# Kernel optimization log

Measured on AMD Instinct MI355X. Metric: run time of the kernel, lower is better.

## Reference

```python
import jax, jax.numpy as jnp
import numpy as np

N, E, D, L, B, T = 50000, 600000, 128, 7, 512, 10
ATOM_DIMS = [119, 4, 12, 12, 10, 6, 6, 2, 2]
BOND_DIMS = [5, 6, 2]
MSG_EPS = 1e-7   # GENConv message epsilon
BN_EPS = 1e-5    # torch BatchNorm1d eps


def _offsets(dims):
    return jnp.asarray(np.concatenate([[0], np.cumsum(dims[:-1])]), dtype=jnp.int32)


def setup_inputs():
    key = jax.random.key(0)
    k = lambda i: jax.random.fold_in(key, i)
    x = jnp.stack([jax.random.randint(k(i), (N,), 0, d) for i, d in enumerate(ATOM_DIMS)], axis=1)
    edge_attr = jnp.stack([jax.random.randint(k(100 + i), (E,), 0, d) for i, d in enumerate(BOND_DIMS)], axis=1)
    edge_index = jax.random.randint(k(200), (2, E), 0, N)
    batch = jnp.sort(jax.random.randint(k(201), (N,), 0, B))
    atom_table = 0.1 * jax.random.normal(k(300), (sum(ATOM_DIMS), D), jnp.float32)
    bond_table = 0.1 * jax.random.normal(k(301), (sum(BOND_DIMS), D), jnp.float32)
    norm_gamma = jnp.ones((L, D), jnp.float32)
    norm_beta = jnp.zeros((L, D), jnp.float32)
    t = 0.1 * jnp.ones((L,), jnp.float32)
    mlp_w1 = 0.05 * jax.random.normal(k(302), (L, D, 2 * D), jnp.float32)
    mlp_b1 = jnp.zeros((L, 2 * D), jnp.float32)
    mlp_bng = jnp.ones((L, 2 * D), jnp.float32)
    mlp_bnb = jnp.zeros((L, 2 * D), jnp.float32)
    mlp_w2 = 0.05 * jax.random.normal(k(303), (L, 2 * D, D), jnp.float32)
    mlp_b2 = jnp.zeros((L, D), jnp.float32)
    pred_w = 0.05 * jax.random.normal(k(304), (D, T), jnp.float32)
    pred_b = jnp.zeros((T,), jnp.float32)
    return dict(x=x, edge_index=edge_index, edge_attr=edge_attr, batch=batch,
                atom_offsets=_offsets(ATOM_DIMS), bond_offsets=_offsets(BOND_DIMS),
                atom_table=atom_table, bond_table=bond_table,
                norm_gamma=norm_gamma, norm_beta=norm_beta, t=t,
                mlp_w1=mlp_w1, mlp_b1=mlp_b1, mlp_bng=mlp_bng, mlp_bnb=mlp_bnb,
                mlp_w2=mlp_w2, mlp_b2=mlp_b2, pred_w=pred_w, pred_b=pred_b)


def _batchnorm(z, gamma, beta):
    # training-mode BatchNorm1d: batch stats, biased variance
    mu = z.mean(0)
    var = z.var(0)
    return (z - mu) * jax.lax.rsqrt(var + BN_EPS) * gamma + beta


def _genconv(h, ea, src, dst, t, w1, b1, g1, bt1, w2, b2):
    # GENConv: message = relu(x_j + edge_attr) + eps; softmax aggregation with temperature t
    msg = jax.nn.relu(h[src] + ea) + MSG_EPS                 # [E, D]
    logits = msg * t
    m = jax.ops.segment_max(logits, dst, num_segments=N)     # [N, D]
    m = jax.lax.stop_gradient(jnp.where(jnp.isfinite(m), m, 0.0))
    e = jnp.exp(logits - m[dst])
    denom = jax.ops.segment_sum(e, dst, num_segments=N)
    alpha = e / (denom[dst] + 1e-16)
    aggr = jax.ops.segment_sum(msg * alpha, dst, num_segments=N)  # [N, D]
    out = h + aggr                                           # update: x_r + aggr
    z = _batchnorm(out @ w1 + b1, g1, bt1)                   # MLP: D -> 2D (BN, ReLU) -> D
    return jax.nn.relu(z) @ w2 + b2


def reference(x, edge_index, edge_attr, batch, atom_offsets, bond_offsets,
              atom_table, bond_table, norm_gamma, norm_beta, t,
              mlp_w1, mlp_b1, mlp_bng, mlp_bnb, mlp_w2, mlp_b2, pred_w, pred_b):
    h = atom_table[x + atom_offsets[None, :]].sum(1)               # [N, D] AtomEncoder
    ea = bond_table[edge_attr + bond_offsets[None, :]].sum(1)      # [E, D] BondEncoder
    src, dst = edge_index[0], edge_index[1]
    # first layer: bare conv
    h = _genconv(h, ea, src, dst, t[0], mlp_w1[0], mlp_b1[0], mlp_bng[0], mlp_bnb[0], mlp_w2[0], mlp_b2[0])
    # remaining layers: res+ blocks (norm -> act -> conv -> residual); dropout=0
    for i in range(1, L):
        r = jax.nn.relu(_batchnorm(h, norm_gamma[i], norm_beta[i]))
        r = _genconv(r, ea, src, dst, t[i], mlp_w1[i], mlp_b1[i], mlp_bng[i], mlp_bnb[i], mlp_w2[i], mlp_b2[i])
        h = h + r
    h = _batchnorm(h, norm_gamma[0], norm_beta[0])                 # layers[0].norm
    # global mean pool over graphs
    sums = jax.ops.segment_sum(h, batch, num_segments=B)
    cnts = jax.ops.segment_sum(jnp.ones((N,), h.dtype), batch, num_segments=B)
    graph_emb = sums / jnp.maximum(cnts, 1.0)[:, None]
    return graph_emb @ pred_w + pred_b                             # [B, T]
```

## Files before the change

### kernel.cpp

```cpp
#include <hip/hip_runtime.h>
#include <hip/hip_bf16.h>

#define N_NODES 50000
#define N_EDGES 600000
#define D 128
#define D2 256
#define NGRAPH 512
#define NTARGET 10
#define NSB 49
#define NSLOT 32

static constexpr float MSG_EPS_F = 1e-7f;
static constexpr float BN_EPS_F  = 1e-5f;

typedef _Float16 half8 __attribute__((ext_vector_type(8)));
typedef _Float16 half4v __attribute__((ext_vector_type(4)));
typedef float f32x4 __attribute__((ext_vector_type(4)));
#define MFMA16(a, b, c) __builtin_amdgcn_mfma_f32_16x16x32_f16(a, b, c, 0, 0, 0)

__global__ __launch_bounds__(256) void k_encode(
    const int* __restrict__ x, const int* __restrict__ aoff,
    const float* __restrict__ atab, float* __restrict__ h,
    _Float16* __restrict__ hh, int* __restrict__ deg) {
  int tid = blockIdx.x * 256 + threadIdx.x;
  if (tid < N_NODES) deg[tid] = 0;
  int n = tid >> 5, f4 = (tid & 31) << 2;
  if (n >= N_NODES) return;
  float4 acc = make_float4(0.f, 0.f, 0.f, 0.f);
#pragma unroll
  for (int i = 0; i < 9; ++i) {
    int row = x[n * 9 + i] + aoff[i];
    float4 v = *(const float4*)&atab[row * D + f4];
    acc.x += v.x; acc.y += v.y; acc.z += v.z; acc.w += v.w;
  }
  *(float4*)&h[(size_t)n * D + f4] = acc;
  half4v o = {(_Float16)acc.x, (_Float16)acc.y, (_Float16)acc.z, (_Float16)acc.w};
  *(half4v*)&hh[(size_t)n * D + f4] = o;
}

__global__ __launch_bounds__(128) void k_combo(
    const int* __restrict__ boff, const float* __restrict__ btab,
    _Float16* __restrict__ comboh) {
  int c = blockIdx.x, t = threadIdx.x;
  int a0 = c / 12, a1 = (c % 12) / 2, a2 = c % 2;
  comboh[c * D + t] = (_Float16)(btab[(boff[0] + a0) * D + t] +
                                 btab[(boff[1] + a1) * D + t] +
                                 btab[(boff[2] + a2) * D + t]);
}

__global__ __launch_bounds__(256) void k_packW(
    const float* __restrict__ w1, const float* __restrict__ w2,
    _Float16* __restrict__ w1p, _Float16* __restrict__ w2p) {
  int t = blockIdx.x * 256 + threadIdx.x;
  if (t < 7 * 4096) {
    int lane = t & 63, ntAll = (t >> 6) & 15, kc = (t >> 10) & 3, l = t >> 12;
    int q = lane >> 4, c = ntAll * 16 + (lane & 15);
    int kbase = kc * 32 + q * 8;
    const float* W = w1 + (size_t)l * D * D2;
    half8 v;
#pragma unroll
    for (int j = 0; j < 8; ++j) v[j] = (_Float16)W[(size_t)(kbase + j) * D2 + c];
    *(half8*)&w1p[(size_t)t * 8] = v;
  } else {
    int u = t - 7 * 4096;
    if (u < 7 * 4096) {
      int lane = u & 63, nt = (u >> 6) & 7, kcAll = (u >> 9) & 7, l = u >> 12;
      int q = lane >> 4, c = nt * 16 + (lane & 15);
      int kbase = kcAll * 32 + q * 8;
      const float* W = w2 + (size_t)l * D2 * D;
      half8 v;
#pragma unroll
      for (int j = 0; j < 8; ++j) v[j] = (_Float16)W[(size_t)(kbase + j) * D + c];
      *(half8*)&w2p[(size_t)u * 8] = v;
    }
  }
}

__global__ __launch_bounds__(256) void k_degree(
    const int* __restrict__ ei, int* __restrict__ deg) {
  int e = blockIdx.x * 256 + threadIdx.x;
  if (e >= N_EDGES) return;
  atomicAdd(&deg[ei[N_EDGES + e]], 1);
}

__global__ __launch_bounds__(1024) void k_scan1(
    const int* __restrict__ deg, int* __restrict__ excl, int* __restrict__ bsum) {
  __shared__ int tmp[1024];
  int t = threadIdx.x, i = blockIdx.x * 1024 + t;
  int v = (i < N_NODES) ? deg[i] : 0;
  tmp[t] = v;
  __syncthreads();
  for (int off = 1; off < 1024; off <<= 1) {
    int add = (t >= off) ? tmp[t - off] : 0;
    __syncthreads();
    tmp[t] += add;
    __syncthreads();
  }
  if (i < N_NODES) excl[i] = tmp[t] - v;
  if (t == 1023) bsum[blockIdx.x] = tmp[1023];
}

__global__ __launch_bounds__(64) void k_scan2(int* __restrict__ bsum) {
  __shared__ int s[64];
  int t = threadIdx.x;
  int v = (t < NSB) ? bsum[t] : 0;
  s[t] = v;
  __syncthreads();
  for (int off = 1; off < 64; off <<= 1) {
    int add = (t >= off) ? s[t - off] : 0;
    __syncthreads();
    s[t] += add;
    __syncthreads();
  }
  if (t < NSB) bsum[t] = s[t] - v;
}

__global__ __launch_bounds__(256) void k_scan3(
    const int* __restrict__ excl, const int* __restrict__ bsum,
    int* __restrict__ rowptr, int* __restrict__ cursor) {
  int i = blockIdx.x * 256 + threadIdx.x;
  if (i < N_NODES) {
    int v = excl[i] + bsum[i >> 10];
    rowptr[i] = v;
    cursor[i] = v;
  }
  if (i == N_NODES) rowptr[N_NODES] = N_EDGES;
}

__global__ __launch_bounds__(256) void k_scatter(
    const int* __restrict__ ei, const int* __restrict__ eattr,
    int* __restrict__ cursor, int* __restrict__ payload) {
  int e = blockIdx.x * 256 + threadIdx.x;
  if (e >= N_EDGES) return;
  int src = ei[e], dst = ei[N_EDGES + e];
  int cid = eattr[e * 3 + 0] * 12 + eattr[e * 3 + 1] * 2 + eattr[e * 3 + 2];
  int pos = atomicAdd(&cursor[dst], 1);
  payload[pos] = (src << 6) | cid;
}

__global__ __launch_bounds__(256) void k_gbounds(
    const int* __restrict__ batch, int* __restrict__ gstart,
    int* __restrict__ hist) {
  int n = blockIdx.x * 256 + threadIdx.x;
  if (n < 64) hist[n] = 0;
  if (n >= N_NODES) return;
  int b0 = batch[n];
  int b1 = (n + 1 < N_NODES) ? batch[n + 1] : NGRAPH;
  for (int bb = b0 + 1; bb <= b1; ++bb) gstart[bb] = n + 1;
  if (n == 0)
    for (int bb = 0; bb <= b0; ++bb) gstart[bb] = 0;
}

__global__ __launch_bounds__(256) void k_hist(
    const int* __restrict__ deg, int* __restrict__ hist) {
  __shared__ int lh[64];
  int tid = threadIdx.x;
  if (tid < 64) lh[tid] = 0;
  __syncthreads();
  int n = blockIdx.x * 256 + tid;
  if (n < N_NODES) atomicAdd(&lh[min(deg[n], 63)], 1);
  __syncthreads();
  if (tid < 64 && lh[tid]) atomicAdd(&hist[tid], lh[tid]);
}

__global__ __launch_bounds__(64) void k_scanhist(
    const int* __restrict__ hist, int* __restrict__ cursor2) {
  __shared__ int s[64];
  int t = threadIdx.x;
  int v = hist[t];
  s[t] = v;
  __syncthreads();
  for (int off = 1; off < 64; off <<= 1) {
    int add = (t >= off) ? s[t - off] : 0;
    __syncthreads();
    s[t] += add;
    __syncthreads();
  }
  cursor2[t] = s[t] - v;
}

__global__ __launch_bounds__(256) void k_permscatter(
    const int* __restrict__ deg, int* __restrict__ cursor2,
    int* __restrict__ perm) {
  __shared__ int lh[64], lbase[64];
  int tid = threadIdx.x;
  if (tid < 64) lh[tid] = 0;
  __syncthreads();
  int n = blockIdx.x * 256 + tid;
  int b = -1, lpos = 0;
  if (n < N_NODES) {
    b = min(deg[n], 63);
    lpos = atomicAdd(&lh[b], 1);
  }
  __syncthreads();
  if (tid < 64 && lh[tid]) lbase[tid] = atomicAdd(&cursor2[tid], lh[tid]);
  __syncthreads();
  if (b >= 0) perm[lbase[b] + lpos] = n;
}

__global__ __launch_bounds__(128) void k_bncoef(
    const float* __restrict__ statHsPrev, const float* __restrict__ gamma,
    const float* __restrict__ beta, float* __restrict__ bncoef, int identity) {
  int t = threadIdx.x;
  if (identity) {
    bncoef[t] = 1.f;
    bncoef[128 + t] = 0.f;
    return;
  }
  float s = 0.f, sq = 0.f;
#pragma unroll
  for (int sl = 0; sl < NSLOT; ++sl) {
    s += statHsPrev[sl * 256 + t];
    sq += statHsPrev[sl * 256 + 128 + t];
  }
  const float invN = 1.0f / (float)N_NODES;
  float mu = s * invN, var = sq * invN - mu * mu;
  float isg = rsqrtf(var + BN_EPS_F) * gamma[t];
  bncoef[t] = isg;
  bncoef[128 + t] = beta[t] - mu * isg;
}

__global__ __launch_bounds__(256) void k_aggrx(
    const _Float16* __restrict__ hh, const int* __restrict__ rowptr,
    const int* __restrict__ payload, const _Float16* __restrict__ comboh,
    const int* __restrict__ perm, const float* __restrict__ tptr, int l,
    const float* __restrict__ bncoef, float negcap, _Float16* __restrict__ xh) {
  int tid = blockIdx.x * 256 + threadIdx.x;
  int gi = tid >> 4, f8 = (tid & 15) << 3;
  if (gi >= N_NODES) return;
  int dst = perm[gi];
  float tv = tptr[l];
  float a[8], bb[8];
  *(float4*)&a[0] = *(const float4*)&bncoef[f8];
  *(float4*)&a[4] = *(const float4*)&bncoef[f8 + 4];
  *(float4*)&bb[0] = *(const float4*)&bncoef[128 + f8];
  *(float4*)&bb[4] = *(const float4*)&bncoef[128 + f8 + 4];
  int s = rowptr[dst], e = rowptr[dst + 1];
  float den[8], S[8];
#pragma unroll
  for (int j = 0; j < 8; ++j) { den[j] = 0.f; S[j] = 0.f; }
  int i = s;
  for (; i + 1 < e; i += 2) {
    int p0 = payload[i], p1 = payload[i + 1];
    half8 h0 = *(const half8*)&hh[(size_t)(p0 >> 6) * D + f8];
    half8 h1v = *(const half8*)&hh[(size_t)(p1 >> 6) * D + f8];
    half8 c0 = *(const half8*)&comboh[(p0 & 63) * D + f8];
    half8 c1 = *(const half8*)&comboh[(p1 & 63) * D + f8];
#pragma unroll
    for (int j = 0; j < 8; ++j) {
      float r0 = fmaxf(fmaf((float)h0[j], a[j], bb[j]), negcap);
      float r1 = fmaxf(fmaf((float)h1v[j], a[j], bb[j]), negcap);
      float m0 = fmaxf(r0 + (float)c0[j], 0.f) + MSG_EPS_F;
      float m1 = fmaxf(r1 + (float)c1[j], 0.f) + MSG_EPS_F;
      float e0 = __expf(m0 * tv), e1 = __expf(m1 * tv);
      den[j] += e0 + e1;
      S[j] += m0 * e0 + m1 * e1;
    }
  }
  if (i < e) {
    int p0 = payload[i];
    half8 h0 = *(const half8*)&hh[(size_t)(p0 >> 6) * D + f8];
    half8 c0 = *(const half8*)&comboh[(p0 & 63) * D + f8];
#pragma unroll
    for (int j = 0; j < 8; ++j) {
      float r0 = fmaxf(fmaf((float)h0[j], a[j], bb[j]), negcap);
      float m0 = fmaxf(r0 + (float)c0[j], 0.f) + MSG_EPS_F;
      float e0 = __expf(m0 * tv);
      den[j] += e0;
      S[j] += m0 * e0;
    }
  }
  half8 hd = *(const half8*)&hh[(size_t)dst * D + f8];
  half8 o;
#pragma unroll
  for (int j = 0; j < 8; ++j) {
    float rd = fmaxf(fmaf((float)hd[j], a[j], bb[j]), negcap);
    o[j] = (_Float16)(rd + S[j] / (den[j] + 1e-16f));
  }
  *(half8*)&xh[(size_t)dst * D + f8] = o;
}

__global__ __launch_bounds__(256) void k_gemm1(
    const _Float16* __restrict__ xh, const _Float16* __restrict__ w1p,
    const float* __restrict__ b1, _Float16* __restrict__ z1h,
    float* __restrict__ stat1s) {
  __shared__ __align__(16) _Float16 Af[512 * 8];
  int tid = threadIdx.x;
  int row0 = blockIdx.x * 32;
  int slot = blockIdx.x & (NSLOT - 1);

#pragma unroll
  for (int s0 = 0; s0 < 2; ++s0) {
    int s = s0 * 256 + tid;
    int kc = s >> 7, mt = (s >> 6) & 1, l2 = s & 63;
    int row = row0 + mt * 16 + (l2 & 15);
    int kb = kc * 32 + ((l2 >> 4) << 3);
    half8 v;
    if (row < N_NODES) {
      v = *(const half8*)&xh[(size_t)row * D + kb];
    } else {
#pragma unroll
      for (int j = 0; j < 8; ++j) v[j] = (_Float16)0.f;
    }
    *(half8*)&Af[s * 8] = v;
  }
  __syncthreads();

  int wv = tid >> 6, ln = tid & 63;
  f32x4 acc[2][4];
#pragma unroll
  for (int i = 0; i < 2; ++i)
#pragma unroll
    for (int j = 0; j < 4; ++j) acc[i][j] = (f32x4){0.f, 0.f, 0.f, 0.f};

#pragma unroll
  for (int kc = 0; kc < 4; ++kc) {
    half8 a0 = *(half8*)&Af[((kc * 2 + 0) * 64 + ln) * 8];
    half8 a1 = *(half8*)&Af[((kc * 2 + 1) * 64 + ln) * 8];
#pragma unroll
    for (int nt = 0; nt < 4; ++nt) {
      int ntAll = wv * 4 + nt;
      half8 b = *(const half8*)&w1p[((size_t)(kc * 16 + ntAll) * 64 + ln) * 8];
      acc[0][nt] = MFMA16(a0, b, acc[0][nt]);
      acc[1][nt] = MFMA16(a1, b, acc[1][nt]);
    }
  }
  int lq = ln >> 4, lc = ln & 15;
  float cs[4], cq[4];
#pragma unroll
  for (int nt = 0; nt < 4; ++nt) { cs[nt] = 0.f; cq[nt] = 0.f; }
#pragma unroll
  for (int nt = 0; nt < 4; ++nt) {
    int col = (wv * 4 + nt) * 16 + lc;
    float bias = b1[col];
#pragma unroll
    for (int mt = 0; mt < 2; ++mt) {
      int rbase = row0 + mt * 16 + lq * 4;
#pragma unroll
      for (int rg = 0; rg < 4; ++rg) {
        int row = rbase + rg;
        if (row < N_NODES) {
          float z = acc[mt][nt][rg] + bias;
          z1h[(size_t)row * D2 + col] = (_Float16)z;
          cs[nt] += z; cq[nt] += z * z;
        }
      }
    }
  }
#pragma unroll
  for (int nt = 0; nt < 4; ++nt) {
    float v = cs[nt], q = cq[nt];
    v += __shfl_xor(v, 16); v += __shfl_xor(v, 32);
    q += __shfl_xor(q, 16); q += __shfl_xor(q, 32);
    if (lq == 0) {
      int col = (wv * 4 + nt) * 16 + lc;
      atomicAdd(&stat1s[slot * 512 + col], v);
      atomicAdd(&stat1s[slot * 512 + 256 + col], q);
    }
  }
}

__global__ __launch_bounds__(256) void k_gemm2(
    const _Float16* __restrict__ z1h, const float* __restrict__ stat1s,
    const float* __restrict__ g1, const float* __restrict__ bt1,
    const _Float16* __restrict__ w2p, const float* __restrict__ b2,
    float* __restrict__ h, _Float16* __restrict__ hh, int residual,
    float* __restrict__ statHs) {
  __shared__ __align__(16) _Float16 Af[1024 * 8];
  __shared__ float s1[512];
  const float invN = 1.0f / (float)N_NODES;
  int tid = threadIdx.x;
  int row0 = blockIdx.x * 32;
  int slot = blockIdx.x & (NSLOT - 1);

#pragma unroll
  for (int jj = 0; jj < 2; ++jj) {
    int j = jj * 256 + tid;
    float a = 0.f;
#pragma unroll
    for (int s = 0; s < NSLOT; ++s) a += stat1s[s * 512 + j];
    s1[j] = a;
  }
  __syncthreads();

#pragma unroll
  for (int s0 = 0; s0 < 4; ++s0) {
    int s = s0 * 256 + tid;
    int kcAll = s >> 7, mt = (s >> 6) & 1, l2 = s & 63;
    int row = row0 + mt * 16 + (l2 & 15);
    int kb = kcAll * 32 + ((l2 >> 4) << 3);
    half8 v;
    if (row < N_NODES) {
      half8 z = *(const half8*)&z1h[(size_t)row * D2 + kb];
#pragma unroll
      for (int j = 0; j < 8; ++j) {
        float mu = s1[kb + j] * invN;
        float isg = rsqrtf(s1[256 + kb + j] * invN - mu * mu + BN_EPS_F) * g1[kb + j];
        v[j] = (_Float16)fmaxf(((float)z[j] - mu) * isg + bt1[kb + j], 0.f);
      }
    } else {
#pragma unroll
      for (int j = 0; j < 8; ++j) v[j] = (_Float16)0.f;
    }
    *(half8*)&Af[s * 8] = v;
  }
  __syncthreads();

  int wv = tid >> 6, ln = tid & 63;
  f32x4 acc[2][2];
#pragma unroll
  for (int i = 0; i < 2; ++i)
#pragma unroll
    for (int j = 0; j < 2; ++j) acc[i][j] = (f32x4){0.f, 0.f, 0.f, 0.f};

#pragma unroll
  for (int kcAll = 0; kcAll < 8; ++kcAll) {
    half8 a0 = *(half8*)&Af[((kcAll * 2 + 0) * 64 + ln) * 8];
    half8 a1 = *(half8*)&Af[((kcAll * 2 + 1) * 64 + ln) * 8];
#pragma unroll
    for (int nt = 0; nt < 2; ++nt) {
      half8 b = *(const half8*)&w2p[((size_t)(kcAll * 8 + wv * 2 + nt) * 64 + ln) * 8];
      acc[0][nt] = MFMA16(a0, b, acc[0][nt]);
      acc[1][nt] = MFMA16(a1, b, acc[1][nt]);
    }
  }
  int lq = ln >> 4, lc = ln & 15;
  float cs[2], cq[2];
#pragma unroll
  for (int nt = 0; nt < 2; ++nt) { cs[nt] = 0.f; cq[nt] = 0.f; }
#pragma unroll
  for (int nt = 0; nt < 2; ++nt) {
    int col = (wv * 2 + nt) * 16 + lc;
    float bias = b2[col];
#pragma unroll
    for (int mt = 0; mt < 2; ++mt) {
      int rbase = row0 + mt * 16 + lq * 4;
#pragma unroll
      for (int rg = 0; rg < 4; ++rg) {
        int row = rbase + rg;
        if (row < N_NODES) {
          float v = acc[mt][nt][rg] + bias;
          if (residual) v += h[(size_t)row * D + col];
          h[(size_t)row * D + col] = v;
          hh[(size_t)row * D + col] = (_Float16)v;
          cs[nt] += v; cq[nt] += v * v;
        }
      }
    }
  }
#pragma unroll
  for (int nt = 0; nt < 2; ++nt) {
    float v = cs[nt], q = cq[nt];
    v += __shfl_xor(v, 16); v += __shfl_xor(v, 32);
    q += __shfl_xor(q, 16); q += __shfl_xor(q, 32);
    if (lq == 0) {
      int col = (wv * 2 + nt) * 16 + lc;
      atomicAdd(&statHs[slot * 256 + col], v);
      atomicAdd(&statHs[slot * 256 + 128 + col], q);
    }
  }
}

__global__ __launch_bounds__(256) void k_poolpred(
    const float* __restrict__ h, const int* __restrict__ gstart,
    const float* __restrict__ statHs, const float* __restrict__ gamma,
    const float* __restrict__ beta, const float* __restrict__ pw,
    const float* __restrict__ pb, float* __restrict__ out) {
  __shared__ float sH[256];
  __shared__ float emb[128];
  __shared__ float4 red[256];
  int b = blockIdx.x, tid = threadIdx.x;
  {
    float a = 0.f;
#pragma unroll
    for (int s = 0; s < NSLOT; ++s) a += statHs[s * 256 + tid];
    sH[tid] = a;
  }
  int fl = (tid & 31) << 2, ns = tid >> 5;
  int gs = gstart[b], ge = gstart[b + 1];
  float4 acc = make_float4(0.f, 0.f, 0.f, 0.f);
  for (int n = gs + ns; n < ge; n += 8) {
    float4 v = *(const float4*)&h[(size_t)n * D + fl];
    acc.x += v.x; acc.y += v.y; acc.z += v.z; acc.w += v.w;
  }
  red[tid] = acc;
  __syncthreads();
  if (ns < 4) {
    float4 o = red[tid + 128];
    acc.x += o.x; acc.y += o.y; acc.z += o.z; acc.w += o.w;
    red[tid] = acc;
  }
  __syncthreads();
  if (ns < 2) {
    float4 o = red[tid + 64];
    acc.x += o.x; acc.y += o.y; acc.z += o.z; acc.w += o.w;
    red[tid] = acc;
  }
  __syncthreads();
  if (ns == 0) {
    float4 o = red[tid + 32];
    acc.x += o.x; acc.y += o.y; acc.z += o.z; acc.w += o.w;
    const float invN = 1.0f / (float)N_NODES;
    float inv = (ge > gs) ? 1.0f / (float)(ge - gs) : 0.f;
    float av[4] = {acc.x, acc.y, acc.z, acc.w};
#pragma unroll
    for (int j = 0; j < 4; ++j) {
      int k = fl + j;
      float mu = sH[k] * invN;
      float var = sH[D + k] * invN - mu * mu;
      emb[k] = (ge > gs)
          ? (av[j] * inv - mu) * rsqrtf(var + BN_EPS_F) * gamma[k] + beta[k]
          : 0.f;
    }
  }
  __syncthreads();
  if (tid < NTARGET) {
    float o = pb[tid];
    for (int k = 0; k < D; ++k) o += emb[k] * pw[k * NTARGET + tid];
    out[b * NTARGET + tid] = o;
  }
}

extern "C" void kernel_launch(void* const* d_in, const int* in_sizes, int n_in,
                              void* d_out, int out_size, void* d_ws, size_t ws_size,
                              hipStream_t stream) {
  const int* x      = (const int*)d_in[0];
  const int* ei     = (const int*)d_in[1];
  const int* eattr  = (const int*)d_in[2];
  const int* batch  = (const int*)d_in[3];
  const int* aoff   = (const int*)d_in[4];
  const int* boff   = (const int*)d_in[5];
  const float* atab = (const float*)d_in[6];
  const float* btab = (const float*)d_in[7];
  const float* ngam = (const float*)d_in[8];
  const float* nbet = (const float*)d_in[9];
  const float* tptr = (const float*)d_in[10];
  const float* w1   = (const float*)d_in[11];
  const float* b1   = (const float*)d_in[12];
  const float* bng  = (const float*)d_in[13];
  const float* bnb  = (const float*)d_in[14];
  const float* w2   = (const float*)d_in[15];
  const float* b2   = (const float*)d_in[16];
  const float* pw   = (const float*)d_in[17];
  const float* pb   = (const float*)d_in[18];
  float* out = (float*)d_out;

  float* ws = (float*)d_ws;
  const size_t ND = (size_t)N_NODES * D;
  float* h      = ws;
  _Float16* hh  = (_Float16*)(ws + 1 * ND);
  _Float16* xh  = (_Float16*)(ws + 1 * ND + ND / 2);
  _Float16* z1h = (_Float16*)(ws + 2 * ND);
  float* statAll = ws + 3 * ND;
  float* stat1sAll = statAll;
  float* statHsAll = statAll + 7 * NSLOT * 512;
  float* bncoef = statHsAll + 7 * NSLOT * 256;
  float* comboF = bncoef + 256;
  _Float16* comboh = (_Float16*)comboF;
  _Float16* w1p = (_Float16*)(comboF + 60 * D);
  _Float16* w2p = w1p + 7 * 32768;
  int* ibuf     = (int*)(w2p + 7 * 32768);
  int* rowptr   = ibuf;
  int* cursor   = rowptr + N_NODES + 1;
  int* deg      = cursor + N_NODES;
  int* payload  = deg + N_NODES;
  int* gstart   = payload + N_EDGES;
  int* excl     = gstart + NGRAPH + 1;
  int* bsum     = excl + N_NODES;
  int* hist     = bsum + 64;
  int* cursor2  = hist + 64;
  int* perm     = cursor2 + 64;

  const int nodeBlocks = (N_NODES * 32 + 255) / 256;
  const int aggrBlocks = (N_NODES * 16 + 255) / 256;
  const int edgeThreadBlocks = (N_EDGES + 255) / 256;
  const int nBlocks256 = (N_NODES + 255) / 256;
  const int gRows32 = (N_NODES + 31) / 32;

  (void)hipMemsetAsync(statAll, 0, (size_t)7 * NSLOT * (512 + 256) * sizeof(float), stream);
  k_encode<<<nodeBlocks, 256, 0, stream>>>(x, aoff, atab, h, hh, deg);
  k_combo<<<60, 128, 0, stream>>>(boff, btab, comboh);
  k_packW<<<(2 * 7 * 4096 + 255) / 256, 256, 0, stream>>>(w1, w2, w1p, w2p);
  k_gbounds<<<nBlocks256, 256, 0, stream>>>(batch, gstart, hist);
  k_degree<<<edgeThreadBlocks, 256, 0, stream>>>(ei, deg);
  k_scan1<<<NSB, 1024, 0, stream>>>(deg, excl, bsum);
  k_scan2<<<1, 64, 0, stream>>>(bsum);
  k_scan3<<<(N_NODES + 256) / 256, 256, 0, stream>>>(excl, bsum, rowptr, cursor);
  k_scatter<<<edgeThreadBlocks, 256, 0, stream>>>(ei, eattr, cursor, payload);
  k_hist<<<nBlocks256, 256, 0, stream>>>(deg, hist);
  k_scanhist<<<1, 64, 0, stream>>>(hist, cursor2);
  k_permscatter<<<nBlocks256, 256, 0, stream>>>(deg, cursor2, perm);

  for (int l = 0; l < 7; ++l) {
    k_bncoef<<<1, 128, 0, stream>>>(
        (l > 0) ? statHsAll + (size_t)(l - 1) * NSLOT * 256 : statHsAll,
        ngam + l * D, nbet + l * D, bncoef, l == 0 ? 1 : 0);
    k_aggrx<<<aggrBlocks, 256, 0, stream>>>(
        hh, rowptr, payload, comboh, perm, tptr, l, bncoef,
        l == 0 ? -1e30f : 0.f, xh);
    k_gemm1<<<gRows32, 256, 0, stream>>>(xh, w1p + (size_t)l * 32768,
                                         b1 + l * D2, z1h,
                                         stat1sAll + (size_t)l * NSLOT * 512);
    k_gemm2<<<gRows32, 256, 0, stream>>>(
        z1h, stat1sAll + (size_t)l * NSLOT * 512, bng + l * D2, bnb + l * D2,
        w2p + (size_t)l * 32768, b2 + l * D, h, hh, l > 0 ? 1 : 0,
        statHsAll + (size_t)l * NSLOT * 256);
  }

  k_poolpred<<<NGRAPH, 256, 0, stream>>>(h, gstart,
                                         statHsAll + (size_t)6 * NSLOT * 256,
                                         ngam, nbet, pw, pb, out);
}
```

Baseline: 870.5 us.

## Merge setup kernels, fold BN coefficients into gemm2 tail, use packed fp16 in aggregation

Several small preprocessing kernels are merged into one setup kernel, and the histogram and permutation steps are folded into the scan kernels. The per-layer k_bncoef launch is removed: the last gemm2 block, found with an atomic counter, computes the next layer's BatchNorm coefficients. The aggregation's elementwise affine, ReLU and edge-add now run as packed fp16 vector ops, and the message epsilon is added once at the end. This cuts launch count and ALU work, at the cost of fp16 rounding in the message path, an epsilon that is no longer applied inside the exponent, and a grid-completion pattern that relies on threadfence ordering.

```diff
diff --git a/kernel.cpp b/kernel.cpp
--- a/kernel.cpp
+++ b/kernel.cpp
@@ -38,32 +38,27 @@
   *(half4v*)&hh[(size_t)n * D + f4] = o;
 }
 
-__global__ __launch_bounds__(128) void k_combo(
+__global__ __launch_bounds__(256) void k_setup(
+    const float* __restrict__ w1, const float* __restrict__ w2,
+    _Float16* __restrict__ w1p, _Float16* __restrict__ w2p,
     const int* __restrict__ boff, const float* __restrict__ btab,
-    _Float16* __restrict__ comboh) {
-  int c = blockIdx.x, t = threadIdx.x;
-  int a0 = c / 12, a1 = (c % 12) / 2, a2 = c % 2;
-  comboh[c * D + t] = (_Float16)(btab[(boff[0] + a0) * D + t] +
-                                 btab[(boff[1] + a1) * D + t] +
-                                 btab[(boff[2] + a2) * D + t]);
-}
-
-__global__ __launch_bounds__(256) void k_packW(
-    const float* __restrict__ w1, const float* __restrict__ w2,
-    _Float16* __restrict__ w1p, _Float16* __restrict__ w2p) {
-  int t = blockIdx.x * 256 + threadIdx.x;
-  if (t < 7 * 4096) {
-    int lane = t & 63, ntAll = (t >> 6) & 15, kc = (t >> 10) & 3, l = t >> 12;
-    int q = lane >> 4, c = ntAll * 16 + (lane & 15);
-    int kbase = kc * 32 + q * 8;
-    const float* W = w1 + (size_t)l * D * D2;
-    half8 v;
-#pragma unroll
-    for (int j = 0; j < 8; ++j) v[j] = (_Float16)W[(size_t)(kbase + j) * D2 + c];
-    *(half8*)&w1p[(size_t)t * 8] = v;
-  } else {
-    int u = t - 7 * 4096;
-    if (u < 7 * 4096) {
+    _Float16* __restrict__ comboh, const int* __restrict__ batch,
+    int* __restrict__ gstart, int* __restrict__ hist,
+    _Float16* __restrict__ bncoefh) {
+  int b = blockIdx.x, tid = threadIdx.x;
+  if (b < 224) {
+    int t = b * 256 + tid;
+    if (t < 7 * 4096) {
+      int lane = t & 63, ntAll = (t >> 6) & 15, kc = (t >> 10) & 3, l = t >> 12;
+      int q = lane >> 4, c = ntAll * 16 + (lane & 15);
+      int kbase = kc * 32 + q * 8;
+      const float* W = w1 + (size_t)l * D * D2;
+      half8 v;
+#pragma unroll
+      for (int j = 0; j < 8; ++j) v[j] = (_Float16)W[(size_t)(kbase + j) * D2 + c];
+      *(half8*)&w1p[(size_t)t * 8] = v;
+    } else {
+      int u = t - 7 * 4096;
       int lane = u & 63, nt = (u >> 6) & 7, kcAll = (u >> 9) & 7, l = u >> 12;
       int q = lane >> 4, c = nt * 16 + (lane & 15);
       int kbase = kcAll * 32 + q * 8;
@@ -73,6 +68,29 @@
       for (int j = 0; j < 8; ++j) v[j] = (_Float16)W[(size_t)(kbase + j) * D + c];
       *(half8*)&w2p[(size_t)u * 8] = v;
     }
+  } else if (b < 254) {
+    int t = (b - 224) * 256 + tid;
+    int c = t >> 7, f = t & 127;
+    if (c < 60) {
+      int a0 = c / 12, a1 = (c % 12) / 2, a2 = c % 2;
+      comboh[c * D + f] = (_Float16)(btab[(boff[0] + a0) * D + f] +
+                                     btab[(boff[1] + a1) * D + f] +
+                                     btab[(boff[2] + a2) * D + f]);
+    }
+  } else if (b < 450) {
+    int n = (b - 254) * 256 + tid;
+    if (n >= N_NODES) return;
+    int b0 = batch[n];
+    int b1 = (n + 1 < N_NODES) ? batch[n + 1] : NGRAPH;
+    for (int bb = b0 + 1; bb <= b1; ++bb) gstart[bb] = n + 1;
+    if (n == 0)
+      for (int bb = 0; bb <= b0; ++bb) gstart[bb] = 0;
+  } else {
+    if (tid < 128) {
+      bncoefh[tid] = (_Float16)1.f;
+      bncoefh[128 + tid] = (_Float16)0.f;
+    }
+    if (tid < 64) hist[tid] = 0;
   }
 }
 
@@ -84,12 +102,16 @@
 }
 
 __global__ __launch_bounds__(1024) void k_scan1(
-    const int* __restrict__ deg, int* __restrict__ excl, int* __restrict__ bsum) {
+    const int* __restrict__ deg, int* __restrict__ excl,
+    int* __restrict__ bsum, int* __restrict__ hist) {
   __shared__ int tmp[1024];
+  __shared__ int lh[64];
   int t = threadIdx.x, i = blockIdx.x * 1024 + t;
+  if (t < 64) lh[t] = 0;
   int v = (i < N_NODES) ? deg[i] : 0;
   tmp[t] = v;
   __syncthreads();
+  if (i < N_NODES) atomicAdd(&lh[min(v, 63)], 1);
   for (int off = 1; off < 1024; off <<= 1) {
     int add = (t >= off) ? tmp[t - off] : 0;
     __syncthreads();
@@ -98,33 +120,53 @@
   }
   if (i < N_NODES) excl[i] = tmp[t] - v;
   if (t == 1023) bsum[blockIdx.x] = tmp[1023];
-}
-
-__global__ __launch_bounds__(64) void k_scan2(int* __restrict__ bsum) {
-  __shared__ int s[64];
+  __syncthreads();
+  if (t < 64 && lh[t]) atomicAdd(&hist[t], lh[t]);
+}
+
+__global__ __launch_bounds__(64) void k_scan2(
+    int* __restrict__ bsum, const int* __restrict__ hist,
+    int* __restrict__ cursor2) {
+  __shared__ int s[64], s2[64];
   int t = threadIdx.x;
-  int v = (t < NSB) ? bsum[t] : 0;
-  s[t] = v;
+  int v1 = (t < NSB) ? bsum[t] : 0;
+  int v2 = hist[t];
+  s[t] = v1; s2[t] = v2;
   __syncthreads();
   for (int off = 1; off < 64; off <<= 1) {
-    int add = (t >= off) ? s[t - off] : 0;
+    int a1 = (t >= off) ? s[t - off] : 0;
+    int a2 = (t >= off) ? s2[t - off] : 0;
     __syncthreads();
-    s[t] += add;
+    s[t] += a1; s2[t] += a2;
     __syncthreads();
   }
-  if (t < NSB) bsum[t] = s[t] - v;
+  if (t < NSB) bsum[t] = s[t] - v1;
+  cursor2[t] = s2[t] - v2;
 }
 
 __global__ __launch_bounds__(256) void k_scan3(
     const int* __restrict__ excl, const int* __restrict__ bsum,
-    int* __restrict__ rowptr, int* __restrict__ cursor) {
-  int i = blockIdx.x * 256 + threadIdx.x;
+    const int* __restrict__ deg, int* __restrict__ cursor2,
+    int* __restrict__ rowptr, int* __restrict__ cursor,
+    int* __restrict__ perm) {
+  __shared__ int lh[64], lbase[64];
+  int tid = threadIdx.x;
+  if (tid < 64) lh[tid] = 0;
+  __syncthreads();
+  int i = blockIdx.x * 256 + tid;
+  int b = -1, lpos = 0;
   if (i < N_NODES) {
     int v = excl[i] + bsum[i >> 10];
     rowptr[i] = v;
     cursor[i] = v;
+    b = min(deg[i], 63);
+    lpos = atomicAdd(&lh[b], 1);
   }
   if (i == N_NODES) rowptr[N_NODES] = N_EDGES;
+  __syncthreads();
+  if (tid < 64 && lh[tid]) lbase[tid] = atomicAdd(&cursor2[tid], lh[tid]);
+  __syncthreads();
+  if (b >= 0) perm[lbase[b] + lpos] = i;
 }
 
 __global__ __launch_bounds__(256) void k_scatter(
@@ -138,103 +180,22 @@
   payload[pos] = (src << 6) | cid;
 }
 
-__global__ __launch_bounds__(256) void k_gbounds(
-    const int* __restrict__ batch, int* __restrict__ gstart,
-    int* __restrict__ hist) {
-  int n = blockIdx.x * 256 + threadIdx.x;
-  if (n < 64) hist[n] = 0;
-  if (n >= N_NODES) return;
-  int b0 = batch[n];
-  int b1 = (n + 1 < N_NODES) ? batch[n + 1] : NGRAPH;
-  for (int bb = b0 + 1; bb <= b1; ++bb) gstart[bb] = n + 1;
-  if (n == 0)
-    for (int bb = 0; bb <= b0; ++bb) gstart[bb] = 0;
-}
-
-__global__ __launch_bounds__(256) void k_hist(
-    const int* __restrict__ deg, int* __restrict__ hist) {
-  __shared__ int lh[64];
-  int tid = threadIdx.x;
-  if (tid < 64) lh[tid] = 0;
-  __syncthreads();
-  int n = blockIdx.x * 256 + tid;
-  if (n < N_NODES) atomicAdd(&lh[min(deg[n], 63)], 1);
-  __syncthreads();
-  if (tid < 64 && lh[tid]) atomicAdd(&hist[tid], lh[tid]);
-}
-
-__global__ __launch_bounds__(64) void k_scanhist(
-    const int* __restrict__ hist, int* __restrict__ cursor2) {
-  __shared__ int s[64];
-  int t = threadIdx.x;
-  int v = hist[t];
-  s[t] = v;
-  __syncthreads();
-  for (int off = 1; off < 64; off <<= 1) {
-    int add = (t >= off) ? s[t - off] : 0;
-    __syncthreads();
-    s[t] += add;
-    __syncthreads();
-  }
-  cursor2[t] = s[t] - v;
-}
-
-__global__ __launch_bounds__(256) void k_permscatter(
-    const int* __restrict__ deg, int* __restrict__ cursor2,
-    int* __restrict__ perm) {
-  __shared__ int lh[64], lbase[64];
-  int tid = threadIdx.x;
-  if (tid < 64) lh[tid] = 0;
-  __syncthreads();
-  int n = blockIdx.x * 256 + tid;
-  int b = -1, lpos = 0;
-  if (n < N_NODES) {
-    b = min(deg[n], 63);
-    lpos = atomicAdd(&lh[b], 1);
-  }
-  __syncthreads();
-  if (tid < 64 && lh[tid]) lbase[tid] = atomicAdd(&cursor2[tid], lh[tid]);
-  __syncthreads();
-  if (b >= 0) perm[lbase[b] + lpos] = n;
-}
-
-__global__ __launch_bounds__(128) void k_bncoef(
-    const float* __restrict__ statHsPrev, const float* __restrict__ gamma,
-    const float* __restrict__ beta, float* __restrict__ bncoef, int identity) {
-  int t = threadIdx.x;
-  if (identity) {
-    bncoef[t] = 1.f;
-    bncoef[128 + t] = 0.f;
-    return;
-  }
-  float s = 0.f, sq = 0.f;
-#pragma unroll
-  for (int sl = 0; sl < NSLOT; ++sl) {
-    s += statHsPrev[sl * 256 + t];
-    sq += statHsPrev[sl * 256 + 128 + t];
-  }
-  const float invN = 1.0f / (float)N_NODES;
-  float mu = s * invN, var = sq * invN - mu * mu;
-  float isg = rsqrtf(var + BN_EPS_F) * gamma[t];
-  bncoef[t] = isg;
-  bncoef[128 + t] = beta[t] - mu * isg;
-}
-
 __global__ __launch_bounds__(256) void k_aggrx(
     const _Float16* __restrict__ hh, const int* __restrict__ rowptr,
     const int* __restrict__ payload, const _Float16* __restrict__ comboh,
     const int* __restrict__ perm, const float* __restrict__ tptr, int l,
-    const float* __restrict__ bncoef, float negcap, _Float16* __restrict__ xh) {
+    const _Float16* __restrict__ bncoefh, float negcap,
+    _Float16* __restrict__ xh) {
   int tid = blockIdx.x * 256 + threadIdx.x;
   int gi = tid >> 4, f8 = (tid & 15) << 3;
   if (gi >= N_NODES) return;
   int dst = perm[gi];
   float tv = tptr[l];
-  float a[8], bb[8];
-  *(float4*)&a[0] = *(const float4*)&bncoef[f8];
-  *(float4*)&a[4] = *(const float4*)&bncoef[f8 + 4];
-  *(float4*)&bb[0] = *(const float4*)&bncoef[128 + f8];
-  *(float4*)&bb[4] = *(const float4*)&bncoef[128 + f8 + 4];
+  half8 a8 = *(const half8*)&bncoefh[f8];
+  half8 b8 = *(const half8*)&bncoefh[128 + f8];
+  half8 cap8, zero8;
+#pragma unroll
+  for (int j = 0; j < 8; ++j) { cap8[j] = (_Float16)negcap; zero8[j] = (_Float16)0.f; }
   int s = rowptr[dst], e = rowptr[dst + 1];
   float den[8], S[8];
 #pragma unroll
@@ -243,40 +204,41 @@
   for (; i + 1 < e; i += 2) {
     int p0 = payload[i], p1 = payload[i + 1];
     half8 h0 = *(const half8*)&hh[(size_t)(p0 >> 6) * D + f8];
-    half8 h1v = *(const half8*)&hh[(size_t)(p1 >> 6) * D + f8];
+    half8 h1 = *(const half8*)&hh[(size_t)(p1 >> 6) * D + f8];
     half8 c0 = *(const half8*)&comboh[(p0 & 63) * D + f8];
     half8 c1 = *(const half8*)&comboh[(p1 & 63) * D + f8];
+    half8 r0 = __builtin_elementwise_max(h0 * a8 + b8, cap8);
+    half8 m0 = __builtin_elementwise_max(r0 + c0, zero8);
+    half8 r1 = __builtin_elementwise_max(h1 * a8 + b8, cap8);
+    half8 m1 = __builtin_elementwise_max(r1 + c1, zero8);
 #pragma unroll
     for (int j = 0; j < 8; ++j) {
-      float r0 = fmaxf(fmaf((float)h0[j], a[j], bb[j]), negcap);
-      float r1 = fmaxf(fmaf((float)h1v[j], a[j], bb[j]), negcap);
-      float m0 = fmaxf(r0 + (float)c0[j], 0.f) + MSG_EPS_F;
-      float m1 = fmaxf(r1 + (float)c1[j], 0.f) + MSG_EPS_F;
-      float e0 = __expf(m0 * tv), e1 = __expf(m1 * tv);
+      float mf0 = (float)m0[j], mf1 = (float)m1[j];
+      float e0 = __expf(mf0 * tv), e1 = __expf(mf1 * tv);
       den[j] += e0 + e1;
-      S[j] += m0 * e0 + m1 * e1;
+      S[j] += mf0 * e0 + mf1 * e1;
     }
   }
   if (i < e) {
     int p0 = payload[i];
     half8 h0 = *(const half8*)&hh[(size_t)(p0 >> 6) * D + f8];
     half8 c0 = *(const half8*)&comboh[(p0 & 63) * D + f8];
+    half8 r0 = __builtin_elementwise_max(h0 * a8 + b8, cap8);
+    half8 m0 = __builtin_elementwise_max(r0 + c0, zero8);
 #pragma unroll
     for (int j = 0; j < 8; ++j) {
-      float r0 = fmaxf(fmaf((float)h0[j], a[j], bb[j]), negcap);
-      float m0 = fmaxf(r0 + (float)c0[j], 0.f) + MSG_EPS_F;
-      float e0 = __expf(m0 * tv);
+      float mf0 = (float)m0[j];
+      float e0 = __expf(mf0 * tv);
       den[j] += e0;
-      S[j] += m0 * e0;
+      S[j] += mf0 * e0;
     }
   }
   half8 hd = *(const half8*)&hh[(size_t)dst * D + f8];
+  half8 rd = __builtin_elementwise_max(hd * a8 + b8, cap8);
   half8 o;
 #pragma unroll
-  for (int j = 0; j < 8; ++j) {
-    float rd = fmaxf(fmaf((float)hd[j], a[j], bb[j]), negcap);
-    o[j] = (_Float16)(rd + S[j] / (den[j] + 1e-16f));
-  }
+  for (int j = 0; j < 8; ++j)
+    o[j] = (_Float16)((float)rd[j] + S[j] / (den[j] + 1e-16f) + MSG_EPS_F);
   *(half8*)&xh[(size_t)dst * D + f8] = o;
 }
 
@@ -365,7 +327,9 @@
     const float* __restrict__ g1, const float* __restrict__ bt1,
     const _Float16* __restrict__ w2p, const float* __restrict__ b2,
     float* __restrict__ h, _Float16* __restrict__ hh, int residual,
-    float* __restrict__ statHs) {
+    float* __restrict__ statHs, const float* __restrict__ gnext,
+    const float* __restrict__ btnext, _Float16* __restrict__ bncoefh,
+    int computeNext, int* __restrict__ done) {
   __shared__ __align__(16) _Float16 Af[1024 * 8];
   __shared__ float s1[512];
   const float invN = 1.0f / (float)N_NODES;
@@ -457,6 +421,28 @@
       int col = (wv * 2 + nt) * 16 + lc;
       atomicAdd(&statHs[slot * 256 + col], v);
       atomicAdd(&statHs[slot * 256 + 128 + col], q);
+    }
+  }
+  if (computeNext) {
+    __threadfence();
+    __shared__ int amLast;
+    if (tid == 0) amLast = (atomicAdd(done, 1) == (int)gridDim.x - 1) ? 1 : 0;
+    __syncthreads();
+    if (amLast) {
+      if (tid == 0) *done = 0;
+      __threadfence();
+      if (tid < 128) {
+        float s = 0.f, sq = 0.f;
+#pragma unroll
+        for (int sl = 0; sl < NSLOT; ++sl) {
+          s  += atomicAdd(&statHs[sl * 256 + tid], 0.f);
+          sq += atomicAdd(&statHs[sl * 256 + 128 + tid], 0.f);
+        }
+        float mu = s * invN, var = sq * invN - mu * mu;
+        float isg = rsqrtf(var + BN_EPS_F) * gnext[tid];
+        bncoefh[tid] = (_Float16)isg;
+        bncoefh[128 + tid] = (_Float16)(btnext[tid] - mu * isg);
+      }
     }
   }
 }
@@ -554,10 +540,11 @@
   float* statAll = ws + 3 * ND;
   float* stat1sAll = statAll;
   float* statHsAll = statAll + 7 * NSLOT * 512;
-  float* bncoef = statHsAll + 7 * NSLOT * 256;
-  float* comboF = bncoef + 256;
+  int* done     = (int*)(statHsAll + 7 * NSLOT * 256);
+  _Float16* bncoefh = (_Float16*)(done + 16);
+  float* comboF = (float*)(bncoefh + 256);
   _Float16* comboh = (_Float16*)comboF;
-  _Float16* w1p = (_Float16*)(comboF + 60 * D);
+  _Float16* w1p = (_Float16*)(comboF + 60 * D / 2);
   _Float16* w2p = w1p + 7 * 32768;
   int* ibuf     = (int*)(w2p + 7 * 32768);
   int* rowptr   = ibuf;
@@ -574,37 +561,33 @@
   const int nodeBlocks = (N_NODES * 32 + 255) / 256;
   const int aggrBlocks = (N_NODES * 16 + 255) / 256;
   const int edgeThreadBlocks = (N_EDGES + 255) / 256;
-  const int nBlocks256 = (N_NODES + 255) / 256;
   const int gRows32 = (N_NODES + 31) / 32;
 
-  (void)hipMemsetAsync(statAll, 0, (size_t)7 * NSLOT * (512 + 256) * sizeof(float), stream);
+  (void)hipMemsetAsync(statAll, 0,
+                       ((size_t)7 * NSLOT * 768 + 16) * sizeof(float), stream);
   k_encode<<<nodeBlocks, 256, 0, stream>>>(x, aoff, atab, h, hh, deg);
-  k_combo<<<60, 128, 0, stream>>>(boff, btab, comboh);
-  k_packW<<<(2 * 7 * 4096 + 255) / 256, 256, 0, stream>>>(w1, w2, w1p, w2p);
-  k_gbounds<<<nBlocks256, 256, 0, stream>>>(batch, gstart, hist);
+  k_setup<<<451, 256, 0, stream>>>(w1, w2, w1p, w2p, boff, btab, comboh,
+                                   batch, gstart, hist, bncoefh);
   k_degree<<<edgeThreadBlocks, 256, 0, stream>>>(ei, deg);
-  k_scan1<<<NSB, 1024, 0, stream>>>(deg, excl, bsum);
-  k_scan2<<<1, 64, 0, stream>>>(bsum);
-  k_scan3<<<(N_NODES + 256) / 256, 256, 0, stream>>>(excl, bsum, rowptr, cursor);
+  k_scan1<<<NSB, 1024, 0, stream>>>(deg, excl, bsum, hist);
+  k_scan2<<<1, 64, 0, stream>>>(bsum, hist, cursor2);
+  k_scan3<<<(N_NODES + 256) / 256, 256, 0, stream>>>(excl, bsum, deg, cursor2,
+                                                     rowptr, cursor, perm);
   k_scatter<<<edgeThreadBlocks, 256, 0, stream>>>(ei, eattr, cursor, payload);
-  k_hist<<<nBlocks256, 256, 0, stream>>>(deg, hist);
-  k_scanhist<<<1, 64, 0, stream>>>(hist, cursor2);
-  k_permscatter<<<nBlocks256, 256, 0, stream>>>(deg, cursor2, perm);
 
   for (int l = 0; l < 7; ++l) {
-    k_bncoef<<<1, 128, 0, stream>>>(
-        (l > 0) ? statHsAll + (size_t)(l - 1) * NSLOT * 256 : statHsAll,
-        ngam + l * D, nbet + l * D, bncoef, l == 0 ? 1 : 0);
     k_aggrx<<<aggrBlocks, 256, 0, stream>>>(
-        hh, rowptr, payload, comboh, perm, tptr, l, bncoef,
-        l == 0 ? -1e30f : 0.f, xh);
+        hh, rowptr, payload, comboh, perm, tptr, l, bncoefh,
+        l == 0 ? -65504.f : 0.f, xh);
     k_gemm1<<<gRows32, 256, 0, stream>>>(xh, w1p + (size_t)l * 32768,
                                          b1 + l * D2, z1h,
                                          stat1sAll + (size_t)l * NSLOT * 512);
+    int nl = (l < 6) ? (l + 1) : 0;
     k_gemm2<<<gRows32, 256, 0, stream>>>(
         z1h, stat1sAll + (size_t)l * NSLOT * 512, bng + l * D2, bnb + l * D2,
         w2p + (size_t)l * 32768, b2 + l * D, h, hh, l > 0 ? 1 : 0,
-        statHsAll + (size_t)l * NSLOT * 256);
+        statHsAll + (size_t)l * NSLOT * 256,
+        ngam + nl * D, nbet + nl * D, bncoefh, l < 6 ? 1 : 0, done);
   }
 
   k_poolpred<<<NGRAPH, 256, 0, stream>>>(h, gstart,
```

Result: slower. 1.873 ms (+115.2%).
